# Kernel tuning notes

Measured on AMD Instinct MI355X. Metric: run time of the kernel, lower is better.

The kernel has to match this reference:

```python
import jax, jax.numpy as jnp
import numpy as np

# MANO fingertip / palm prior vertex indices from contact_loss
_F1 = [697,698,699,700,712,713,714,715,737,738,739,740,741,743,744,745,746,748,749,750,753,754,755,756,757,758,759,760,761,762,763,764,765,766,767,768]
_F2 = [46,47,48,49,164,165,166,167,194,195,223,237,238,280,281,298,301,317,320,323,324,325,326,327,328,329,330,331,332,333,340,341,342,343,344,345,346,347,348,349,350,351,352,353,354,355]
_F3 = [356,357,358,359,375,376,386,387,396,397,402,403,413,429,433,434,435,436,437,438,439,440,441,442,443,444,452,453,454,455,456,459,460,461,462,463,464,465,466,467]
_F4 = [468,469,470,471,484,485,486,496,497,506,507,513,514,524,545,546,547,548,549,550,551,552,553,555,563,564,565,566,567,570,572,573,574,575,576,577,578]
_F5 = [580,581,582,583,600,601,602,614,615,624,625,630,631,641,663,664,665,666,667,668,670,672,680,681,682,683,684,686,687,688,689,690,691,692,693,694,695]
_F0 = [73,96,98,99,772,774,775,777]
PRIOR_IDX = np.array(_F1 + _F2 + _F3 + _F4 + _F5 + _F0, dtype=np.int32)

KL_COEF = 0.005
A_W, B_W, C_W, D_W, E_W = 1.0, 0.1, 1000.0, 10.0, 10.0  # init kwargs a..e


def _nn(src, trg):
    """Brute-force 1-NN: src [B,N1,3] -> trg [B,N2,3].
    Returns (sq_dist [B,N1], idx [B,N1], diff src-near [B,N1,3])."""
    d2 = (jnp.sum(src * src, -1)[:, :, None]
          + jnp.sum(trg * trg, -1)[:, None, :]
          - 2.0 * jnp.einsum('bnd,bmd->bnm', src, trg))  # [B,N1,N2]
    idx = jnp.argmin(d2, axis=-1)
    near = jnp.take_along_axis(trg, idx[:, :, None], axis=1)
    diff = src - near
    return jnp.sum(diff * diff, axis=-1), idx, diff


def _p2p_signed(x, y, x_normals):
    """point2point_signed(x, y, x_normals): signed dist y->x, unsigned x->y."""
    _, yidx, y2x = _nn(y, x)  # nearest x for each y
    y_nn_normal = jnp.take_along_axis(x_normals, yidx[:, :, None], axis=1)
    in_out = jnp.sign(jnp.sum(y_nn_normal * y2x, axis=-1))
    y2x_signed = jnp.sqrt(jnp.sum(y2x * y2x, axis=-1)) * in_out  # [B,P2]
    _, _, x2y = _nn(x, y)  # nearest y for each x
    x2y_dist = jnp.sqrt(jnp.sum(x2y * x2y, axis=-1))  # [B,P1]
    return y2x_signed, x2y_dist


def _forward(recon_xyz, gt_xyz, recon_normals, gt_normals, obj_xyz, mean, log_var, v_weights):
    B = recon_xyz.shape[0]
    f32 = recon_xyz.dtype
    # --- CVAE recon (L2) + KLD ---
    recon_loss = jnp.sum((recon_xyz - gt_xyz) ** 2) / B
    kld = -0.5 * jnp.sum(1.0 + log_var - mean ** 2 - jnp.exp(log_var)) / B * 10.0
    # --- obj -> hand NN (squared dists, pytorch3d knn_points convention) ---
    recon_d2, recon_idx, _ = _nn(obj_xyz, recon_xyz)  # [B,3000]
    gt_d2, _, _ = _nn(obj_xyz, gt_xyz)
    # --- contact map from GT NN dist thresholding ---
    cmap = jnp.sqrt(gt_d2) < 0.005  # [B,3000] bool
    # --- contact_loss: obj NN to prior (fingertip/palm) recon verts ---
    prior = recon_xyz[:, PRIOR_IDX, :]
    obj_cd, _, _ = _nn(obj_xyz, prior)
    n_pts = jnp.sum(cmap.astype(f32))
    contact = 3000.0 * jnp.where(n_pts > 0, jnp.sum(obj_cd * cmap) / (B * n_pts), 0.0)
    # --- CMap_consistency_loss ---
    recon_cmap = jnp.sqrt(recon_d2) < 0.005
    consistency = -5.0 * jnp.sum((recon_cmap & cmap).astype(f32)) / (n_pts + 1e-4)
    # --- inter_penetr_loss: interior obj points via NN-normal dot sign ---
    nn_hand = jnp.take_along_axis(recon_xyz, recon_idx[:, :, None], axis=1)
    nn_normal = jnp.take_along_axis(recon_normals, recon_idx[:, :, None], axis=1)
    interior = jnp.sum((nn_hand - obj_xyz) * nn_normal, axis=-1) > 0
    penetr = 100.0 * jnp.sum(recon_d2 * interior) / B
    # --- loss_cnet: signed chamfer consistency ---
    vw2 = v_weights ** (1.0 / 2.5)
    o2h, h2o = _p2p_signed(recon_xyz, obj_xyz, recon_normals)
    o2h_gt, h2o_gt = _p2p_signed(gt_xyz, obj_xyz, gt_normals)
    w_dist = (o2h_gt < 0.01) & (o2h_gt > -0.005)
    w_neg = o2h < 0.0
    w = jnp.where(w_neg, 1.5, jnp.where(w_dist, 1.0, 0.1))
    loss_h = 35.0 * (1.0 - KL_COEF) * jnp.mean(jnp.abs(jnp.abs(h2o) - jnp.abs(h2o_gt)) * vw2)
    loss_o = 30.0 * (1.0 - KL_COEF) * jnp.mean(jnp.abs(o2h - o2h_gt) * w)
    cnet = loss_h + loss_o
    return (A_W * recon_loss + B_W * kld + C_W * penetr
            + D_W * contact + E_W * consistency + cnet)


def setup_inputs() -> dict:
    key = jax.random.key(0)
    ks = jax.random.split(key, 8)
    B, NH, NO, Z = 32, 778, 3000, 64
    s = 0.05  # meter-scale point clouds so contact thresholds (5mm) are meaningful
    def unit(k, shape):
        v = jax.random.normal(k, shape, dtype=jnp.float32)
        return v / jnp.linalg.norm(v, axis=-1, keepdims=True)
    return {
        'recon_xyz': jax.random.normal(ks[0], (B, NH, 3), dtype=jnp.float32) * s,
        'gt_xyz': jax.random.normal(ks[1], (B, NH, 3), dtype=jnp.float32) * s,
        'recon_normals': unit(ks[2], (B, NH, 3)),
        'gt_normals': unit(ks[3], (B, NH, 3)),
        'obj_xyz': jax.random.normal(ks[4], (B, NO, 3), dtype=jnp.float32) * s,
        'mean': jax.random.normal(ks[5], (B, Z), dtype=jnp.float32),
        'log_var': jax.random.normal(ks[6], (B, Z), dtype=jnp.float32) * 0.1,
        'v_weights': jax.random.uniform(ks[7], (NH,), dtype=jnp.float32),
    }


def reference(recon_xyz, gt_xyz, recon_normals, gt_normals, obj_xyz, mean, log_var, v_weights):
    return _forward(recon_xyz, gt_xyz, recon_normals, gt_normals, obj_xyz, mean, log_var, v_weights)
```

## Files before the change

### kernel.cpp

```cpp
#include <hip/hip_runtime.h>
#include <math.h>


#define NB 32
#define NH 778
#define NO 3000
#define NZ 64
#define NP 204

#define P_OBJ 4
#define OBJ_PTS 1024
#define OBJ_TILES 3
#define JSPLIT 4
#define JCH 195
#define HC 12
#define HCS 250
#define OBJ_BLKS (NB * OBJ_TILES * JSPLIT)
#define HAND_BLKS (NB * HC)
#define T2 12
#define FIN_OBJ_BLKS (NB * T2)
#define FIN_TAIL_BLKS ((NB * NH + 255) / 256)
#define FIN_BLKS (FIN_OBJ_BLKS + FIN_TAIL_BLKS)

#define NKEY (NB * NO)
#define NHT  (NB * NH)

typedef unsigned int uint32;

__device__ __constant__ int c_prior[NP] = {
  697,698,699,700,712,713,714,715,737,738,739,740,741,743,744,745,746,748,749,750,
  753,754,755,756,757,758,759,760,761,762,763,764,765,766,767,768,
  46,47,48,49,164,165,166,167,194,195,223,237,238,280,281,298,301,317,320,323,
  324,325,326,327,328,329,330,331,332,333,340,341,342,343,344,345,346,347,348,349,
  350,351,352,353,354,355,
  356,357,358,359,375,376,386,387,396,397,402,403,413,429,433,434,435,436,437,438,
  439,440,441,442,443,444,452,453,454,455,456,459,460,461,462,463,464,465,466,467,
  468,469,470,471,484,485,486,496,497,506,507,513,514,524,545,546,547,548,549,550,
  551,552,553,555,563,564,565,566,567,570,572,573,574,575,576,577,578,
  580,581,582,583,600,601,602,614,615,624,625,630,631,641,663,664,665,666,667,668,
  670,672,680,681,682,683,684,686,687,688,689,690,691,692,693,694,695,
  73,96,98,99,772,774,775,777
};

__device__ __constant__ int c_prior_sorted[NP] = {
  46,47,48,49,73,96,98,99,164,165,166,167,194,
  195,223,237,238,280,281,298,301,317,320,323,324,325,326,327,328,329,330,331,
  332,333,340,341,342,343,344,345,346,347,348,349,350,351,352,353,354,355,356,
  357,358,359,375,376,386,387,
  396,397,402,403,413,429,433,434,435,436,437,438,439,440,441,442,443,444,452,
  453,454,455,456,459,460,461,462,463,464,465,466,467,468,469,470,471,484,485,
  486,496,497,506,507,513,514,524,545,546,547,548,549,550,551,552,553,555,563,
  564,565,566,567,570,572,573,574,575,576,577,578,580,581,582,583,
  600,601,602,614,615,624,625,630,631,641,663,664,665,666,667,668,670,672,680,
  681,682,683,684,686,687,688,689,690,691,692,693,694,695,697,698,699,700,712,
  713,714,715,737,738,739,740,741,743,744,745,746,748,749,750,753,754,755,756,
  757,758,759,760,761,762,763,764,765,766,767,768,772,774,775,777
};
__device__ __constant__ int c_psplit[JSPLIT + 1] = {0, 13, 58, 131, 204};

__device__ inline float wave_sum(float v) {
  v += __shfl_down(v, 32);
  v += __shfl_down(v, 16);
  v += __shfl_down(v, 8);
  v += __shfl_down(v, 4);
  v += __shfl_down(v, 2);
  v += __shfl_down(v, 1);
  return v;
}

__device__ inline float packkey(float t, int j) {
  return __uint_as_float((__float_as_uint(t) & 0xFFFFFC00u) | (uint32)j);
}

__global__ __launch_bounds__(256) void mega1a(
    const float* __restrict__ recon, const float* __restrict__ gt,
    const float* __restrict__ obj,
    float* __restrict__ keyR, float* __restrict__ keyG,
    float* __restrict__ priorK,
    float* __restrict__ minHR, float* __restrict__ minHG,
    float* __restrict__ accs)
{
  const int bid = blockIdx.x;
  const int tid = threadIdx.x;

  if (bid == 0 && tid < 16) accs[tid] = 0.0f;

  if (bid < OBJ_BLKS) {
    __shared__ float4 shA[JCH];
    __shared__ float4 shB[JCH];
    const int b     = bid / (OBJ_TILES * JSPLIT);
    const int rem   = bid % (OBJ_TILES * JSPLIT);
    const int tile  = rem / JSPLIT;
    const int split = rem % JSPLIT;
    const int jbase = split * JCH;
    const int jcnt  = (NH - jbase < JCH) ? (NH - jbase) : JCH;

    for (int i = tid; i < jcnt; i += 256) {
      const float* p = recon + ((size_t)b * NH + jbase + i) * 3;
      float x = p[0], y = p[1], z = p[2];
      shA[i] = make_float4(x, y, z, x*x + y*y + z*z);
      const float* q = gt + ((size_t)b * NH + jbase + i) * 3;
      float gx = q[0], gy = q[1], gz = q[2];
      shB[i] = make_float4(gx, gy, gz, gx*gx + gy*gy + gz*gz);
    }
    __syncthreads();

    float nx[P_OBJ], ny[P_OBJ], nz[P_OBJ];
    int ob[P_OBJ]; bool val[P_OBJ];
    #pragma unroll
    for (int m = 0; m < P_OBJ; ++m) {
      int o = tile * OBJ_PTS + m * 256 + tid;
      ob[m] = o; val[m] = (o < NO);
      float x = 0.f, y = 0.f, z = 0.f;
      if (val[m]) {
        const float* op = obj + ((size_t)b * NO + o) * 3;
        x = op[0]; y = op[1]; z = op[2];
      }
      nx[m] = -2.f * x; ny[m] = -2.f * y; nz[m] = -2.f * z;
    }

    float bR[P_OBJ], bG[P_OBJ];
    #pragma unroll
    for (int m = 0; m < P_OBJ; ++m) { bR[m] = 3.4e38f; bG[m] = 3.4e38f; }

    int i = 0;
    for (; i + 1 < jcnt; i += 2) {
      float4 h0 = shA[i], h1 = shA[i + 1];
      #pragma unroll
      for (int m = 0; m < P_OBJ; ++m) {
        float t0 = fmaf(nx[m], h0.x, h0.w); t0 = fmaf(ny[m], h0.y, t0); t0 = fmaf(nz[m], h0.z, t0);
        float t1 = fmaf(nx[m], h1.x, h1.w); t1 = fmaf(ny[m], h1.y, t1); t1 = fmaf(nz[m], h1.z, t1);
        bR[m] = fminf(bR[m], fminf(packkey(t0, jbase + i), packkey(t1, jbase + i + 1)));
      }
      float4 g0 = shB[i], g1 = shB[i + 1];
      #pragma unroll
      for (int m = 0; m < P_OBJ; ++m) {
        float t0 = fmaf(nx[m], g0.x, g0.w); t0 = fmaf(ny[m], g0.y, t0); t0 = fmaf(nz[m], g0.z, t0);
        float t1 = fmaf(nx[m], g1.x, g1.w); t1 = fmaf(ny[m], g1.y, t1); t1 = fmaf(nz[m], g1.z, t1);
        bG[m] = fminf(bG[m], fminf(packkey(t0, jbase + i), packkey(t1, jbase + i + 1)));
      }
    }
    if (i < jcnt) {
      float4 h0 = shA[i];
      float4 g0 = shB[i];
      #pragma unroll
      for (int m = 0; m < P_OBJ; ++m) {
        float t0 = fmaf(nx[m], h0.x, h0.w); t0 = fmaf(ny[m], h0.y, t0); t0 = fmaf(nz[m], h0.z, t0);
        bR[m] = fminf(bR[m], packkey(t0, jbase + i));
        float u0 = fmaf(nx[m], g0.x, g0.w); u0 = fmaf(ny[m], g0.y, u0); u0 = fmaf(nz[m], g0.z, u0);
        bG[m] = fminf(bG[m], packkey(u0, jbase + i));
      }
    }

    float bP[P_OBJ];
    #pragma unroll
    for (int m = 0; m < P_OBJ; ++m) bP[m] = 3.4e38f;
    const int pk0 = c_psplit[split], pk1 = c_psplit[split + 1];
    for (int k = pk0; k < pk1; ++k) {
      float4 h = shA[c_prior_sorted[k] - jbase];
      #pragma unroll
      for (int m = 0; m < P_OBJ; ++m) {
        float t = fmaf(nx[m], h.x, h.w);
        t = fmaf(ny[m], h.y, t);
        t = fmaf(nz[m], h.z, t);
        bP[m] = fminf(bP[m], t);
      }
    }

    #pragma unroll
    for (int m = 0; m < P_OBJ; ++m) {
      if (!val[m]) continue;
      const size_t idx = (size_t)split * NKEY + (size_t)b * NO + ob[m];
      keyR[idx] = bR[m];
      keyG[idx] = bG[m];
      priorK[idx] = bP[m];
    }
  } else {
    __shared__ float4 sO[HCS];
    const int bid2 = bid - OBJ_BLKS;
    const int oc = bid2 % HC;
    const int b  = bid2 / HC;

    const float* Ob = obj + ((size_t)b * NO + oc * HCS) * 3;
    for (int i2 = tid; i2 < HCS; i2 += 256) {
      float x = Ob[3*i2], y = Ob[3*i2+1], z = Ob[3*i2+2];
      sO[i2] = make_float4(x, y, z, x*x + y*y + z*z);
    }
    __syncthreads();

    float nrx[4], nry[4], nrz[4];
    float ngx[4], ngy[4], ngz[4];
    bool val[4];
    #pragma unroll
    for (int m = 0; m < 4; ++m) {
      int j = m * 256 + tid;
      val[m] = (j < NH);
      float rx = 0.f, ry = 0.f, rz = 0.f, gx = 0.f, gy = 0.f, gz = 0.f;
      if (val[m]) {
        const float* rp = recon + ((size_t)b * NH + j) * 3;
        const float* gp = gt    + ((size_t)b * NH + j) * 3;
        rx = rp[0]; ry = rp[1]; rz = rp[2];
        gx = gp[0]; gy = gp[1]; gz = gp[2];
      }
      nrx[m] = -2.f*rx; nry[m] = -2.f*ry; nrz[m] = -2.f*rz;
      ngx[m] = -2.f*gx; ngy[m] = -2.f*gy; ngz[m] = -2.f*gz;
    }

    float mR[4], mG[4];
    #pragma unroll
    for (int m = 0; m < 4; ++m) { mR[m] = 3.4e38f; mG[m] = 3.4e38f; }

    for (int k = 0; k < HCS; k += 2) {
      float4 o0 = sO[k], o1 = sO[k + 1];
      #pragma unroll
      for (int m = 0; m < 4; ++m) {
        float t0 = fmaf(nrx[m], o0.x, o0.w); t0 = fmaf(nry[m], o0.y, t0); t0 = fmaf(nrz[m], o0.z, t0);
        float t1 = fmaf(nrx[m], o1.x, o1.w); t1 = fmaf(nry[m], o1.y, t1); t1 = fmaf(nrz[m], o1.z, t1);
        mR[m] = fminf(mR[m], fminf(t0, t1));
        float u0 = fmaf(ngx[m], o0.x, o0.w); u0 = fmaf(ngy[m], o0.y, u0); u0 = fmaf(ngz[m], o0.z, u0);
        float u1 = fmaf(ngx[m], o1.x, o1.w); u1 = fmaf(ngy[m], o1.y, u1); u1 = fmaf(ngz[m], o1.z, u1);
        mG[m] = fminf(mG[m], fminf(u0, u1));
      }
    }

    #pragma unroll
    for (int m = 0; m < 4; ++m) {
      if (!val[m]) continue;
      int j = m * 256 + tid;
      const size_t idx = (size_t)oc * NHT + (size_t)b * NH + j;
      minHR[idx] = mR[m];
      minHG[idx] = mG[m];
    }
  }
}

__global__ __launch_bounds__(256) void mega2a(
    const float* __restrict__ recon, const float* __restrict__ gt,
    const float* __restrict__ rnorm, const float* __restrict__ gnorm,
    const float* __restrict__ obj,
    const float* __restrict__ mean, const float* __restrict__ logv,
    const float* __restrict__ vw,
    const float* __restrict__ keyR, const float* __restrict__ keyG,
    const float* __restrict__ priorK,
    const float* __restrict__ minHR, const float* __restrict__ minHG,
    float* __restrict__ accs, float* __restrict__ out)
{
  __shared__ float red[4][5];
  const int bid = blockIdx.x;
  const int tid = threadIdx.x;
  const int lane = tid & 63, wv = tid >> 6;

  if (bid < FIN_OBJ_BLKS) {
    const int b = bid / T2;
    const int tile = bid % T2;
    const int o = tile * 256 + tid;
    float penetr = 0.f, nptsv = 0.f, contactv = 0.f, consistv = 0.f, lossov = 0.f;
    if (o < NO) {
      const float* op = obj + ((size_t)b * NO + o) * 3;
      const float ox = op[0], oy = op[1], oz = op[2];
      const float o2 = ox*ox + oy*oy + oz*oz;
      const size_t base = (size_t)b * NO + o;

      float kR = 3.4e38f, kG = 3.4e38f, bP = 3.4e38f;
      #pragma unroll
      for (int s = 0; s < JSPLIT; ++s) {
        kR = fminf(kR, keyR[(size_t)s * NKEY + base]);
        kG = fminf(kG, keyG[(size_t)s * NKEY + base]);
        bP = fminf(bP, priorK[(size_t)s * NKEY + base]);
      }
      uint32 kRb = __float_as_uint(kR), kGb = __float_as_uint(kG);
      int idxR = (int)(kRb & 0x3FFu), idxG = (int)(kGb & 0x3FFu);
      float d2R = fmaxf(__uint_as_float(kRb & 0xFFFFFC00u) + o2, 0.f);
      float d2G = fmaxf(__uint_as_float(kGb & 0xFFFFFC00u) + o2, 0.f);
      float d2P = fmaxf(bP + o2, 0.f);

      const float* hR = recon + ((size_t)b * NH + idxR) * 3;
      const float* nR = rnorm + ((size_t)b * NH + idxR) * 3;
      float dotR = (ox - hR[0]) * nR[0] + (oy - hR[1]) * nR[1] + (oz - hR[2]) * nR[2];
      const float* hG = gt + ((size_t)b * NH + idxG) * 3;
      const float* nG = gnorm + ((size_t)b * NH + idxG) * 3;
      float dotG = (ox - hG[0]) * nG[0] + (oy - hG[1]) * nG[1] + (oz - hG[2]) * nG[2];

      float sgnR = (dotR > 0.f) ? 1.f : ((dotR < 0.f) ? -1.f : 0.f);
      float sgnG = (dotG > 0.f) ? 1.f : ((dotG < 0.f) ? -1.f : 0.f);
      float sR_ = sqrtf(d2R), sG_ = sqrtf(d2G);
      float o2h = sR_ * sgnR, o2hg = sG_ * sgnG;

      bool interior = dotR < 0.f;
      bool cmap = sG_ < 0.005f;
      bool rcmap = sR_ < 0.005f;

      penetr   = interior ? d2R : 0.f;
      nptsv    = cmap ? 1.f : 0.f;
      contactv = cmap ? d2P : 0.f;
      consistv = (cmap && rcmap) ? 1.f : 0.f;
      float w = (o2h < 0.f) ? 1.5f
              : (((o2hg < 0.01f) && (o2hg > -0.005f)) ? 1.f : 0.1f);
      lossov = fabsf(o2h - o2hg) * w;
    }

    float vals[5] = {penetr, nptsv, contactv, consistv, lossov};
    #pragma unroll
    for (int q = 0; q < 5; ++q) {
      float s = wave_sum(vals[q]);
      if (lane == 0) red[wv][q] = s;
    }
    __syncthreads();
    if (tid < 5) {
      float s = red[0][tid] + red[1][tid] + red[2][tid] + red[3][tid];
      atomicAdd(&accs[tid], s);
    }
  } else {
    const int t = (bid - FIN_OBJ_BLKS) * 256 + tid;
    float lossh = 0.f, rsum = 0.f, ksum = 0.f;
    if (t < NB * NH) {
      const float* rp = recon + (size_t)t * 3;
      const float* gp = gt + (size_t)t * 3;
      float rx = rp[0], ry = rp[1], rz = rp[2];
      float gx = gp[0], gy = gp[1], gz = gp[2];
      float d0 = rx - gx, d1 = ry - gy, d2 = rz - gz;
      rsum = d0*d0 + d1*d1 + d2*d2;

      float tR[HC], tG[HC];
      #pragma unroll
      for (int c = 0; c < HC; ++c) {
        tR[c] = minHR[(size_t)c * NHT + t];
        tG[c] = minHG[(size_t)c * NHT + t];
      }
      float mRt = tR[0], mGt = tG[0];
      #pragma unroll
      for (int c = 1; c < HC; ++c) {
        mRt = fminf(mRt, tR[c]);
        mGt = fminf(mGt, tG[c]);
      }
      float r2 = rx*rx + ry*ry + rz*rz;
      float g2 = gx*gx + gy*gy + gz*gz;
      float d2Rh = fmaxf(mRt + r2, 0.f);
      float d2Gh = fmaxf(mGt + g2, 0.f);
      int j = t % NH;
      lossh = fabsf(sqrtf(d2Rh) - sqrtf(d2Gh)) * powf(vw[j], 0.4f);
    }
    if (t < NB * NZ) {
      float m = mean[t], lv = logv[t];
      ksum = 1.f + lv - m * m - expf(lv);
    }
    float vals[3] = {lossh, rsum, ksum};
    #pragma unroll
    for (int q = 0; q < 3; ++q) {
      float s = wave_sum(vals[q]);
      if (lane == 0) red[wv][q] = s;
    }
    __syncthreads();
    if (tid < 3) {
      float s = red[0][tid] + red[1][tid] + red[2][tid] + red[3][tid];
      atomicAdd(&accs[5 + tid], s);
    }
  }

  __syncthreads();
  if (tid == 0) {
    __threadfence();
    int* cnt = (int*)(accs + 8);
    int old = atomicAdd(cnt, 1);
    if (old == FIN_BLKS - 1) {
      float a[8];
      #pragma unroll
      for (int q = 0; q < 8; ++q) a[q] = atomicAdd(&accs[q], 0.0f);
      const float recon_loss = a[6] / (float)NB;
      const float kld = -0.5f * a[7] / (float)NB * 10.f;
      const float penetr = 100.f * a[0] / (float)NB;
      const float npts = a[1];
      const float contact = (npts > 0.f) ? (3000.f * a[2] / ((float)NB * npts)) : 0.f;
      const float consistency = -5.f * a[3] / (npts + 0.0001f);
      const float lossh = 35.f * (1.f - 0.005f) * (a[5] / (float)(NB * NH));
      const float losso = 30.f * (1.f - 0.005f) * (a[4] / (float)(NB * NO));
      out[0] = recon_loss + 0.1f * kld + 1000.f * penetr + 10.f * contact
             + 10.f * consistency + lossh + losso;
    }
  }
}

__global__ __launch_bounds__(256) void obj_mono(
    const float* __restrict__ recon, const float* __restrict__ gt,
    const float* __restrict__ rnorm, const float* __restrict__ gnorm,
    const float* __restrict__ obj, float* __restrict__ accs)
{
  __shared__ float4 sR[NH];
  __shared__ float4 sG[NH];
  __shared__ float red[4][5];
  const int b = blockIdx.x / 12;
  const int tile = blockIdx.x % 12;
  const int tid = threadIdx.x;
  for (int i = tid; i < NH; i += 256) {
    const float* p = recon + ((size_t)b * NH + i) * 3;
    float x = p[0], y = p[1], z = p[2];
    sR[i] = make_float4(x, y, z, x*x + y*y + z*z);
    const float* q = gt + ((size_t)b * NH + i) * 3;
    float gx = q[0], gy = q[1], gz = q[2];
    sG[i] = make_float4(gx, gy, gz, gx*gx + gy*gy + gz*gz);
  }
  __syncthreads();
  const int o = tile * 256 + tid;
  float penetr = 0.f, nptsv = 0.f, contactv = 0.f, consistv = 0.f, lossov = 0.f;
  if (o < NO) {
    const float* op = obj + ((size_t)b * NO + o) * 3;
    const float ox = op[0], oy = op[1], oz = op[2];
    const float nx = -2.f*ox, ny = -2.f*oy, nz = -2.f*oz;
    const float o2 = ox*ox + oy*oy + oz*oz;
    float bR = 3.4e38f, bG = 3.4e38f; int iR = 0, iG = 0;
    for (int i = 0; i < NH; ++i) {
      float4 h = sR[i];
      float t = fmaf(nx, h.x, h.w); t = fmaf(ny, h.y, t); t = fmaf(nz, h.z, t);
      if (t < bR) { bR = t; iR = i; }
      float4 g = sG[i];
      float u = fmaf(nx, g.x, g.w); u = fmaf(ny, g.y, u); u = fmaf(nz, g.z, u);
      if (u < bG) { bG = u; iG = i; }
    }
    float bP = 3.4e38f;
    for (int k = 0; k < NP; ++k) {
      float4 h = sR[c_prior[k]];
      float t = fmaf(nx, h.x, h.w); t = fmaf(ny, h.y, t); t = fmaf(nz, h.z, t);
      bP = fminf(bP, t);
    }
    float d2R = fmaxf(bR + o2, 0.f);
    float d2G = fmaxf(bG + o2, 0.f);
    float d2P = fmaxf(bP + o2, 0.f);
    float4 hR = sR[iR];
    const float* nR = rnorm + ((size_t)b * NH + iR) * 3;
    float dotR = (ox-hR.x)*nR[0] + (oy-hR.y)*nR[1] + (oz-hR.z)*nR[2];
    float4 hG = sG[iG];
    const float* nG = gnorm + ((size_t)b * NH + iG) * 3;
    float dotG = (ox-hG.x)*nG[0] + (oy-hG.y)*nG[1] + (oz-hG.z)*nG[2];
    float sgnR = (dotR > 0.f) ? 1.f : ((dotR < 0.f) ? -1.f : 0.f);
    float sgnG = (dotG > 0.f) ? 1.f : ((dotG < 0.f) ? -1.f : 0.f);
    float sR_ = sqrtf(d2R), sG_ = sqrtf(d2G);
    float o2h = sR_*sgnR, o2hg = sG_*sgnG;
    bool interior = dotR < 0.f;
    bool cmap = sG_ < 0.005f, rcmap = sR_ < 0.005f;
    penetr = interior ? d2R : 0.f;
    nptsv = cmap ? 1.f : 0.f;
    contactv = cmap ? d2P : 0.f;
    consistv = (cmap && rcmap) ? 1.f : 0.f;
    float w = (o2h < 0.f) ? 1.5f : (((o2hg < 0.01f) && (o2hg > -0.005f)) ? 1.f : 0.1f);
    lossov = fabsf(o2h - o2hg) * w;
  }
  float vals[5] = {penetr, nptsv, contactv, consistv, lossov};
  const int lane = tid & 63, wv = tid >> 6;
  for (int q = 0; q < 5; ++q) {
    float s = wave_sum(vals[q]);
    if (lane == 0) red[wv][q] = s;
  }
  __syncthreads();
  if (tid < 5) {
    float s = red[0][tid] + red[1][tid] + red[2][tid] + red[3][tid];
    atomicAdd(&accs[tid], s);
  }
}

__global__ __launch_bounds__(256) void hand_full(
    const float* __restrict__ recon, const float* __restrict__ gt,
    const float* __restrict__ obj, const float* __restrict__ vw,
    float* __restrict__ accs)
{
  __shared__ float4 sO[500];
  __shared__ float red[4];
  const int b = blockIdx.x >> 2;
  const int j = ((blockIdx.x & 3) << 8) + threadIdx.x;
  const bool valid = j < NH;
  float rx=0,ry=0,rz=0,gx=0,gy=0,gz=0;
  if (valid) {
    const float* rp = recon + ((size_t)b * NH + j) * 3;
    const float* gp = gt + ((size_t)b * NH + j) * 3;
    rx=rp[0];ry=rp[1];rz=rp[2]; gx=gp[0];gy=gp[1];gz=gp[2];
  }
  const float nrx=-2.f*rx, nry=-2.f*ry, nrz=-2.f*rz;
  const float ngx=-2.f*gx, ngy=-2.f*gy, ngz=-2.f*gz;
  const float r2 = rx*rx+ry*ry+rz*rz, g2 = gx*gx+gy*gy+gz*gz;
  float mR = 3.4e38f, mG = 3.4e38f;
  for (int oc = 0; oc < 6; ++oc) {
    __syncthreads();
    const float* Ob = obj + ((size_t)b * NO + oc * 500) * 3;
    for (int i = threadIdx.x; i < 500; i += 256) {
      float x = Ob[3*i], y = Ob[3*i+1], z = Ob[3*i+2];
      sO[i] = make_float4(x, y, z, x*x + y*y + z*z);
    }
    __syncthreads();
    if (valid) {
      for (int k = 0; k < 500; ++k) {
        float4 o4 = sO[k];
        float t = fmaf(nrx,o4.x,o4.w); t = fmaf(nry,o4.y,t); t = fmaf(nrz,o4.z,t);
        mR = fminf(mR, t);
        float u = fmaf(ngx,o4.x,o4.w); u = fmaf(ngy,o4.y,u); u = fmaf(ngz,o4.z,u);
        mG = fminf(mG, u);
      }
    }
  }
  float lossh = valid ? fabsf(sqrtf(fmaxf(mR+r2,0.f)) - sqrtf(fmaxf(mG+g2,0.f))) * powf(vw[j], 0.4f) : 0.f;
  const int lane = threadIdx.x & 63, wv = threadIdx.x >> 6;
  float s = wave_sum(lossh);
  if (lane == 0) red[wv] = s;
  __syncthreads();
  if (threadIdx.x == 0) atomicAdd(&accs[5], red[0]+red[1]+red[2]+red[3]);
}

__global__ __launch_bounds__(256) void tail_nomins(
    const float* __restrict__ recon, const float* __restrict__ gt,
    const float* __restrict__ mean, const float* __restrict__ logv,
    float* __restrict__ accs)
{
  __shared__ float red[4][2];
  const int t = blockIdx.x * 256 + threadIdx.x;
  float rsum = 0.f, ksum = 0.f;
  if (t < NB * NH) {
    const float* rp = recon + (size_t)t * 3;
    const float* gp = gt + (size_t)t * 3;
    float d0 = rp[0]-gp[0], d1 = rp[1]-gp[1], d2 = rp[2]-gp[2];
    rsum = d0*d0 + d1*d1 + d2*d2;
  }
  if (t < NB * NZ) {
    float m = mean[t], lv = logv[t];
    ksum = 1.f + lv - m*m - expf(lv);
  }
  float vals[2] = {rsum, ksum};
  const int lane = threadIdx.x & 63, wv = threadIdx.x >> 6;
  for (int q = 0; q < 2; ++q) {
    float s = wave_sum(vals[q]);
    if (lane == 0) red[wv][q] = s;
  }
  __syncthreads();
  if (threadIdx.x < 2) {
    float s = red[0][threadIdx.x] + red[1][threadIdx.x] + red[2][threadIdx.x] + red[3][threadIdx.x];
    atomicAdd(&accs[6 + threadIdx.x], s);
  }
}

__global__ void init_small(float* accs) {
  int t = threadIdx.x;
  if (t < 8) accs[t] = 0.0f;
}

__global__ void final_fb(const float* __restrict__ a, float* __restrict__ out) {
  const float recon_loss = a[6] / (float)NB;
  const float kld = -0.5f * a[7] / (float)NB * 10.f;
  const float penetr = 100.f * a[0] / (float)NB;
  const float npts = a[1];
  const float contact = (npts > 0.f) ? (3000.f * a[2] / ((float)NB * npts)) : 0.f;
  const float consistency = -5.f * a[3] / (npts + 0.0001f);
  const float lossh = 35.f * (1.f - 0.005f) * (a[5] / (float)(NB * NH));
  const float losso = 30.f * (1.f - 0.005f) * (a[4] / (float)(NB * NO));
  out[0] = recon_loss + 0.1f*kld + 1000.f*penetr + 10.f*contact + 10.f*consistency + lossh + losso;
}

extern "C" void kernel_launch(void* const* d_in, const int* in_sizes, int n_in,
                              void* d_out, int out_size, void* d_ws, size_t ws_size,
                              hipStream_t stream) {
  const float* recon = (const float*)d_in[0];
  const float* gt    = (const float*)d_in[1];
  const float* rnorm = (const float*)d_in[2];
  const float* gnorm = (const float*)d_in[3];
  const float* obj   = (const float*)d_in[4];
  const float* mean  = (const float*)d_in[5];
  const float* logv  = (const float*)d_in[6];
  const float* vw    = (const float*)d_in[7];
  float* out = (float*)d_out;

  float* accs   = (float*)d_ws;
  float* keyR   = (float*)((char*)d_ws + 256);
  float* keyG   = keyR + (size_t)JSPLIT * NKEY;
  float* priorK = keyG + (size_t)JSPLIT * NKEY;
  float* minHR  = priorK + (size_t)JSPLIT * NKEY;
  float* minHG  = minHR + (size_t)HC * NHT;
  const size_t neededA = 256 + (3ull * JSPLIT * NKEY + 2ull * HC * NHT) * sizeof(float);

  if (ws_size >= neededA) {
    mega1a<<<OBJ_BLKS + HAND_BLKS, 256, 0, stream>>>(
        recon, gt, obj, keyR, keyG, priorK, minHR, minHG, accs);
    mega2a<<<FIN_BLKS, 256, 0, stream>>>(
        recon, gt, rnorm, gnorm, obj, mean, logv, vw,
        keyR, keyG, priorK, minHR, minHG, accs, out);
  } else {
    init_small<<<1, 64, 0, stream>>>(accs);
    obj_mono<<<NB * 12, 256, 0, stream>>>(recon, gt, rnorm, gnorm, obj, accs);
    hand_full<<<NB * 4, 256, 0, stream>>>(recon, gt, obj, vw, accs);
    tail_nomins<<<(NB * NH + 255) / 256, 256, 0, stream>>>(recon, gt, mean, logv, accs);
    final_fb<<<1, 1, 0, stream>>>(accs, out);
  }
}
```

Before: 122.7 us.

## Use v_min3/v_and_or inline asm and trim wasted hand-tile work

Replaces the pack-key bit ops and pairwise fminf with single v_and_or_b32 and v_min3_f32 instructions via inline asm in the obj-to-hand scan, prior scan (now unrolled by two) and hand-to-obj scan. The hand blocks now compute 3 full slices of 256 hand points per thread, and the 10-point tail (768..777) is handled by one rotating wave per block instead of every thread carrying a mostly idle fourth slot. This is meant to cut VALU instruction count and the wasted fourth-slot work. It adds inline asm dependencies and a small change to the lossh division order.

```diff
diff --git a/kernel.cpp b/kernel.cpp
--- a/kernel.cpp
+++ b/kernel.cpp
@@ -68,8 +68,15 @@
   return v;
 }
 
-__device__ inline float packkey(float t, int j) {
-  return __uint_as_float((__float_as_uint(t) & 0xFFFFFC00u) | (uint32)j);
+__device__ __forceinline__ float f_min3(float a, float b, float c) {
+  float r;
+  asm("v_min3_f32 %0, %1, %2, %3" : "=v"(r) : "v"(a), "v"(b), "v"(c));
+  return r;
+}
+__device__ __forceinline__ float f_packao(float t, int j, uint32 mask) {
+  float r;
+  asm("v_and_or_b32 %0, %1, %2, %3" : "=v"(r) : "v"(t), "s"(mask), "v"(j));
+  return r;
 }
 
 __global__ __launch_bounds__(256) void mega1a(
@@ -82,6 +89,7 @@
 {
   const int bid = blockIdx.x;
   const int tid = threadIdx.x;
+  const uint32 KMASK = 0xFFFFFC00u;
 
   if (bid == 0 && tid < 16) accs[tid] = 0.0f;
 
@@ -125,30 +133,32 @@
 
     int i = 0;
     for (; i + 1 < jcnt; i += 2) {
+      const int j0 = jbase + i, j1 = jbase + i + 1;
       float4 h0 = shA[i], h1 = shA[i + 1];
+      float4 g0 = shB[i], g1 = shB[i + 1];
       #pragma unroll
       for (int m = 0; m < P_OBJ; ++m) {
         float t0 = fmaf(nx[m], h0.x, h0.w); t0 = fmaf(ny[m], h0.y, t0); t0 = fmaf(nz[m], h0.z, t0);
         float t1 = fmaf(nx[m], h1.x, h1.w); t1 = fmaf(ny[m], h1.y, t1); t1 = fmaf(nz[m], h1.z, t1);
-        bR[m] = fminf(bR[m], fminf(packkey(t0, jbase + i), packkey(t1, jbase + i + 1)));
-      }
-      float4 g0 = shB[i], g1 = shB[i + 1];
+        bR[m] = f_min3(bR[m], f_packao(t0, j0, KMASK), f_packao(t1, j1, KMASK));
+      }
       #pragma unroll
       for (int m = 0; m < P_OBJ; ++m) {
-        float t0 = fmaf(nx[m], g0.x, g0.w); t0 = fmaf(ny[m], g0.y, t0); t0 = fmaf(nz[m], g0.z, t0);
-        float t1 = fmaf(nx[m], g1.x, g1.w); t1 = fmaf(ny[m], g1.y, t1); t1 = fmaf(nz[m], g1.z, t1);
-        bG[m] = fminf(bG[m], fminf(packkey(t0, jbase + i), packkey(t1, jbase + i + 1)));
+        float u0 = fmaf(nx[m], g0.x, g0.w); u0 = fmaf(ny[m], g0.y, u0); u0 = fmaf(nz[m], g0.z, u0);
+        float u1 = fmaf(nx[m], g1.x, g1.w); u1 = fmaf(ny[m], g1.y, u1); u1 = fmaf(nz[m], g1.z, u1);
+        bG[m] = f_min3(bG[m], f_packao(u0, j0, KMASK), f_packao(u1, j1, KMASK));
       }
     }
     if (i < jcnt) {
+      const int j0 = jbase + i;
       float4 h0 = shA[i];
       float4 g0 = shB[i];
       #pragma unroll
       for (int m = 0; m < P_OBJ; ++m) {
         float t0 = fmaf(nx[m], h0.x, h0.w); t0 = fmaf(ny[m], h0.y, t0); t0 = fmaf(nz[m], h0.z, t0);
-        bR[m] = fminf(bR[m], packkey(t0, jbase + i));
+        bR[m] = fminf(bR[m], f_packao(t0, j0, KMASK));
         float u0 = fmaf(nx[m], g0.x, g0.w); u0 = fmaf(ny[m], g0.y, u0); u0 = fmaf(nz[m], g0.z, u0);
-        bG[m] = fminf(bG[m], packkey(u0, jbase + i));
+        bG[m] = fminf(bG[m], f_packao(u0, j0, KMASK));
       }
     }
 
@@ -156,13 +166,22 @@
     #pragma unroll
     for (int m = 0; m < P_OBJ; ++m) bP[m] = 3.4e38f;
     const int pk0 = c_psplit[split], pk1 = c_psplit[split + 1];
-    for (int k = pk0; k < pk1; ++k) {
-      float4 h = shA[c_prior_sorted[k] - jbase];
+    int k = pk0;
+    for (; k + 1 < pk1; k += 2) {
+      float4 ha = shA[c_prior_sorted[k] - jbase];
+      float4 hb = shA[c_prior_sorted[k + 1] - jbase];
       #pragma unroll
       for (int m = 0; m < P_OBJ; ++m) {
-        float t = fmaf(nx[m], h.x, h.w);
-        t = fmaf(ny[m], h.y, t);
-        t = fmaf(nz[m], h.z, t);
+        float t = fmaf(nx[m], ha.x, ha.w); t = fmaf(ny[m], ha.y, t); t = fmaf(nz[m], ha.z, t);
+        float u = fmaf(nx[m], hb.x, hb.w); u = fmaf(ny[m], hb.y, u); u = fmaf(nz[m], hb.z, u);
+        bP[m] = f_min3(bP[m], t, u);
+      }
+    }
+    if (k < pk1) {
+      float4 ha = shA[c_prior_sorted[k] - jbase];
+      #pragma unroll
+      for (int m = 0; m < P_OBJ; ++m) {
+        float t = fmaf(nx[m], ha.x, ha.w); t = fmaf(ny[m], ha.y, t); t = fmaf(nz[m], ha.z, t);
         bP[m] = fminf(bP[m], t);
       }
     }
@@ -188,48 +207,69 @@
     }
     __syncthreads();
 
-    float nrx[4], nry[4], nrz[4];
-    float ngx[4], ngy[4], ngz[4];
-    bool val[4];
-    #pragma unroll
-    for (int m = 0; m < 4; ++m) {
-      int j = m * 256 + tid;
-      val[m] = (j < NH);
-      float rx = 0.f, ry = 0.f, rz = 0.f, gx = 0.f, gy = 0.f, gz = 0.f;
-      if (val[m]) {
-        const float* rp = recon + ((size_t)b * NH + j) * 3;
-        const float* gp = gt    + ((size_t)b * NH + j) * 3;
-        rx = rp[0]; ry = rp[1]; rz = rp[2];
-        gx = gp[0]; gy = gp[1]; gz = gp[2];
-      }
-      nrx[m] = -2.f*rx; nry[m] = -2.f*ry; nrz[m] = -2.f*rz;
-      ngx[m] = -2.f*gx; ngy[m] = -2.f*gy; ngz[m] = -2.f*gz;
-    }
-
-    float mR[4], mG[4];
-    #pragma unroll
-    for (int m = 0; m < 4; ++m) { mR[m] = 3.4e38f; mG[m] = 3.4e38f; }
-
-    for (int k = 0; k < HCS; k += 2) {
-      float4 o0 = sO[k], o1 = sO[k + 1];
-      #pragma unroll
-      for (int m = 0; m < 4; ++m) {
+    float nrx[3], nry[3], nrz[3];
+    float ngx[3], ngy[3], ngz[3];
+    #pragma unroll
+    for (int m = 0; m < 3; ++m) {
+      const int j = m * 256 + tid;
+      const float* rp = recon + ((size_t)b * NH + j) * 3;
+      const float* gp = gt    + ((size_t)b * NH + j) * 3;
+      nrx[m] = -2.f*rp[0]; nry[m] = -2.f*rp[1]; nrz[m] = -2.f*rp[2];
+      ngx[m] = -2.f*gp[0]; ngy[m] = -2.f*gp[1]; ngz[m] = -2.f*gp[2];
+    }
+
+    float mR[3], mG[3];
+    #pragma unroll
+    for (int m = 0; m < 3; ++m) { mR[m] = 3.4e38f; mG[m] = 3.4e38f; }
+
+    for (int k2 = 0; k2 < HCS; k2 += 2) {
+      float4 o0 = sO[k2], o1 = sO[k2 + 1];
+      #pragma unroll
+      for (int m = 0; m < 3; ++m) {
         float t0 = fmaf(nrx[m], o0.x, o0.w); t0 = fmaf(nry[m], o0.y, t0); t0 = fmaf(nrz[m], o0.z, t0);
         float t1 = fmaf(nrx[m], o1.x, o1.w); t1 = fmaf(nry[m], o1.y, t1); t1 = fmaf(nrz[m], o1.z, t1);
-        mR[m] = fminf(mR[m], fminf(t0, t1));
+        mR[m] = f_min3(mR[m], t0, t1);
         float u0 = fmaf(ngx[m], o0.x, o0.w); u0 = fmaf(ngy[m], o0.y, u0); u0 = fmaf(ngz[m], o0.z, u0);
         float u1 = fmaf(ngx[m], o1.x, o1.w); u1 = fmaf(ngy[m], o1.y, u1); u1 = fmaf(ngz[m], o1.z, u1);
-        mG[m] = fminf(mG[m], fminf(u0, u1));
-      }
-    }
-
-    #pragma unroll
-    for (int m = 0; m < 4; ++m) {
-      if (!val[m]) continue;
-      int j = m * 256 + tid;
+        mG[m] = f_min3(mG[m], u0, u1);
+      }
+    }
+
+    #pragma unroll
+    for (int m = 0; m < 3; ++m) {
+      const int j = m * 256 + tid;
       const size_t idx = (size_t)oc * NHT + (size_t)b * NH + j;
       minHR[idx] = mR[m];
       minHG[idx] = mG[m];
+    }
+
+    const int tw = bid2 & 3;
+    if ((tid >> 6) == tw) {
+      const int j3 = 768 + (tid & 63);
+      const bool v3 = (j3 < NH);
+      float rx=0.f,ry=0.f,rz=0.f,gx=0.f,gy=0.f,gz=0.f;
+      if (v3) {
+        const float* rp = recon + ((size_t)b * NH + j3) * 3;
+        const float* gp = gt    + ((size_t)b * NH + j3) * 3;
+        rx=rp[0];ry=rp[1];rz=rp[2]; gx=gp[0];gy=gp[1];gz=gp[2];
+      }
+      const float n3rx=-2.f*rx, n3ry=-2.f*ry, n3rz=-2.f*rz;
+      const float n3gx=-2.f*gx, n3gy=-2.f*gy, n3gz=-2.f*gz;
+      float m3R = 3.4e38f, m3G = 3.4e38f;
+      for (int k2 = 0; k2 < HCS; k2 += 2) {
+        float4 o0 = sO[k2], o1 = sO[k2 + 1];
+        float t0 = fmaf(n3rx, o0.x, o0.w); t0 = fmaf(n3ry, o0.y, t0); t0 = fmaf(n3rz, o0.z, t0);
+        float t1 = fmaf(n3rx, o1.x, o1.w); t1 = fmaf(n3ry, o1.y, t1); t1 = fmaf(n3rz, o1.z, t1);
+        m3R = f_min3(m3R, t0, t1);
+        float u0 = fmaf(n3gx, o0.x, o0.w); u0 = fmaf(n3gy, o0.y, u0); u0 = fmaf(n3gz, o0.z, u0);
+        float u1 = fmaf(n3gx, o1.x, o1.w); u1 = fmaf(n3gy, o1.y, u1); u1 = fmaf(n3gz, o1.z, u1);
+        m3G = f_min3(m3G, u0, u1);
+      }
+      if (v3) {
+        const size_t idx = (size_t)oc * NHT + (size_t)b * NH + j3;
+        minHR[idx] = m3R;
+        minHG[idx] = m3G;
+      }
     }
   }
 }
@@ -546,7 +586,7 @@
   const float npts = a[1];
   const float contact = (npts > 0.f) ? (3000.f * a[2] / ((float)NB * npts)) : 0.f;
   const float consistency = -5.f * a[3] / (npts + 0.0001f);
-  const float lossh = 35.f * (1.f - 0.005f) * (a[5] / (float)(NB * NH));
+  const float lossh = 35.f * (1.f - 0.005f) * (a[5] / (float)NB / (float)NH);
   const float losso = 30.f * (1.f - 0.005f) * (a[4] / (float)(NB * NO));
   out[0] = recon_loss + 0.1f*kld + 1000.f*penetr + 10.f*contact + 10.f*consistency + lossh + losso;
 }
```

Result: no change. 123.8 us (+0.9%).
